# Kernel optimization log

Measured on AMD Instinct MI355X. Metric: run time of the kernel, lower is better.

The kernel has to match this reference:

```python
import jax, jax.numpy as jnp
import numpy as np

N_NODES = 100000
N_EDGES = 1600000
D_IN = 64
D_HID = 64
D_OUT = 64


def _sage_conv(x, src, dst, n_nodes, W_l, b_l, W_r):
    # mean aggregation of source features at destination nodes
    msgs = x[src]  # [E, F] gather
    agg = jax.ops.segment_sum(msgs, dst, num_segments=n_nodes)
    cnt = jax.ops.segment_sum(jnp.ones((src.shape[0],), x.dtype), dst, num_segments=n_nodes)
    mean = agg / jnp.maximum(cnt, 1.0)[:, None]  # nodes with no in-edges -> 0
    # out = lin_l(mean) + lin_r(x); lin_l has bias, lin_r does not (PyG default)
    return mean @ W_l.T + b_l + x @ W_r.T


def setup_inputs() -> dict:
    key = jax.random.key(0)
    ks = jax.random.split(key, 8)
    x = jax.random.normal(ks[0], (N_NODES, D_IN), dtype=jnp.float32)
    edge_index = jax.random.randint(ks[1], (2, N_EDGES), 0, N_NODES, dtype=jnp.int64) if jax.config.jax_enable_x64 else jax.random.randint(ks[1], (2, N_EDGES), 0, N_NODES, dtype=jnp.int32)
    s1 = 1.0 / np.sqrt(D_IN)
    s2 = 1.0 / np.sqrt(D_HID)
    W1_l = jax.random.uniform(ks[2], (D_HID, D_IN), jnp.float32, -s1, s1)
    b1_l = jax.random.uniform(ks[3], (D_HID,), jnp.float32, -s1, s1)
    W1_r = jax.random.uniform(ks[4], (D_HID, D_IN), jnp.float32, -s1, s1)
    W2_l = jax.random.uniform(ks[5], (D_OUT, D_HID), jnp.float32, -s2, s2)
    b2_l = jax.random.uniform(ks[6], (D_OUT,), jnp.float32, -s2, s2)
    W2_r = jax.random.uniform(ks[7], (D_OUT, D_HID), jnp.float32, -s2, s2)
    return {"x": x, "edge_index": edge_index, "W1_l": W1_l, "b1_l": b1_l, "W1_r": W1_r,
            "W2_l": W2_l, "b2_l": b2_l, "W2_r": W2_r}


def reference(x, edge_index, W1_l, b1_l, W1_r, W2_l, b2_l, W2_r):
    src, dst = edge_index[0], edge_index[1]
    h = _sage_conv(x, src, dst, x.shape[0], W1_l, b1_l, W1_r)
    h = jax.nn.relu(h)
    out = _sage_conv(h, src, dst, x.shape[0], W2_l, b2_l, W2_r)
    return out
```

## Files before the change

### kernel.cpp

```cpp
#include <hip/hip_runtime.h>
#include <hip/hip_fp16.h>

#define N_NODES 100000
#define N_EDGES 1600000
#define D 64

#define BSHIFT 8
#define BUCK_N 256
#define NBUCK 391
#define EPB 4096
#define NBLKA 391
#define SCAN_N (NBUCK * NBLKA)
#define SCAN_B1 ((SCAN_N + 255) / 256)
#define A4_CAP 6144
#define X_OCTETS (N_NODES * D / 8)
#define CVT_BLKS ((X_OCTETS + 2048 + 511) / 512)
#define AGB (N_NODES / 32)

typedef _Float16 half8 __attribute__((ext_vector_type(8)));
typedef float floatx4 __attribute__((ext_vector_type(4)));


__device__ __forceinline__ uint4 pack8h(float4 a, float4 b) {
    __half2 h0, h1, h2, h3;
    h0.x = __float2half(a.x); h0.y = __float2half(a.y);
    h1.x = __float2half(a.z); h1.y = __float2half(a.w);
    h2.x = __float2half(b.x); h2.y = __float2half(b.y);
    h3.x = __float2half(b.z); h3.y = __float2half(b.w);
    uint4 pk;
    pk.x = *(unsigned int*)&h0; pk.y = *(unsigned int*)&h1;
    pk.z = *(unsigned int*)&h2; pk.w = *(unsigned int*)&h3;
    return pk;
}


__global__ void pre_k(const float* __restrict__ x,
                      const float* __restrict__ W1l, const float* __restrict__ W1r,
                      const float* __restrict__ W2l, const float* __restrict__ W2r,
                      const int* __restrict__ dst, int* __restrict__ histG,
                      __half* __restrict__ x16,
                      __half* __restrict__ o1l, __half* __restrict__ o1r,
                      __half* __restrict__ o2l, __half* __restrict__ o2r) {
    __shared__ int hl[512];
    int t = threadIdx.x;
    if (blockIdx.x < NBLKA) {
        hl[t] = 0;
        __syncthreads();
        int base = blockIdx.x * EPB;
#pragma unroll
        for (int r = 0; r < 8; r++) {
            int idx = base + r * 512 + t;
            if (idx < N_EDGES) atomicAdd(&hl[dst[idx] >> BSHIFT], 1);
        }
        __syncthreads();
        if (t < NBUCK) histG[t * NBLKA + blockIdx.x] = hl[t];
        return;
    }
    int i = (blockIdx.x - NBLKA) * 512 + t;
    const float* s;
    __half* d;
    int j;
    if (i < X_OCTETS) {
        s = x; d = x16; j = i * 8;
    } else {
        int k = i - X_OCTETS;
        if (k >= 2048) return;
        int arr = k >> 9;
        j = (k & 511) * 8;
        s = (arr == 0) ? W1l : (arr == 1) ? W1r : (arr == 2) ? W2l : W2r;
        d = (arr == 0) ? o1l : (arr == 1) ? o1r : (arr == 2) ? o2l : o2r;
    }
    float4 a = *(const float4*)&s[j];
    float4 b = *(const float4*)&s[j + 4];
    *(uint4*)&d[j] = pack8h(a, b);
}


__global__ void scan1_k(int* __restrict__ data, int* __restrict__ bsums, int n) {
    __shared__ int sm[256];
    int i = blockIdx.x * 256 + threadIdx.x;
    int v = (i < n) ? data[i] : 0;
    sm[threadIdx.x] = v;
    __syncthreads();
    for (int off = 1; off < 256; off <<= 1) {
        int t = (threadIdx.x >= off) ? sm[threadIdx.x - off] : 0;
        __syncthreads();
        sm[threadIdx.x] += t;
        __syncthreads();
    }
    if (i < n) data[i] = sm[threadIdx.x] - v;
    if (threadIdx.x == 255) bsums[blockIdx.x] = sm[255];
}

__global__ void scan2_k(int* __restrict__ bsums, int nb) {
    __shared__ int sm[1024];
    int v = (threadIdx.x < nb) ? bsums[threadIdx.x] : 0;
    sm[threadIdx.x] = v;
    __syncthreads();
    for (int off = 1; off < 1024; off <<= 1) {
        int t = (threadIdx.x >= off) ? sm[threadIdx.x - off] : 0;
        __syncthreads();
        sm[threadIdx.x] += t;
        __syncthreads();
    }
    if (threadIdx.x < nb) bsums[threadIdx.x] = sm[threadIdx.x];
}

__device__ __forceinline__ int hist_abs(const int* histG, const int* bsums, int idx) {
    int v = histG[idx];
    int blk = idx >> 8;
    if (blk > 0) v += bsums[blk - 1];
    return v;
}


__global__ void a3_sort_k(const int* __restrict__ src, const int* __restrict__ dst,
                          const int* __restrict__ histG, const int* __restrict__ bsums,
                          unsigned int* __restrict__ epacked, int e) {
    __shared__ int hl[512];
    __shared__ int cur[512];
    __shared__ int sc[512];
    __shared__ int gbase[NBUCK];
    __shared__ unsigned int spk[EPB];
    __shared__ unsigned short sb[EPB];
    int t = threadIdx.x;
    int blk = blockIdx.x;
    int base = blk * EPB;

    hl[t] = 0;
    __syncthreads();

    int myd[8], mys[8];
#pragma unroll
    for (int r = 0; r < 8; r++) {
        int idx = base + r * 512 + t;
        if (idx < e) {
            myd[r] = dst[idx];
            mys[r] = src[idx];
            atomicAdd(&hl[myd[r] >> BSHIFT], 1);
        } else {
            myd[r] = -1; mys[r] = 0;
        }
    }
    __syncthreads();

    int v = hl[t];
    sc[t] = v;
    __syncthreads();
    for (int off = 1; off < 512; off <<= 1) {
        int tt = (t >= off) ? sc[t - off] : 0;
        __syncthreads();
        sc[t] += tt;
        __syncthreads();
    }
    int excl = sc[t] - v;
    hl[t] = excl;
    cur[t] = excl;
    if (t < NBUCK) gbase[t] = hist_abs(histG, bsums, t * NBLKA + blk);
    __syncthreads();

#pragma unroll
    for (int r = 0; r < 8; r++) {
        if (myd[r] >= 0) {
            int b = myd[r] >> BSHIFT;
            int dl = myd[r] & (BUCK_N - 1);
            int pos = atomicAdd(&cur[b], 1);
            spk[pos] = ((unsigned)dl << 17) | (unsigned)mys[r];
            sb[pos] = (unsigned short)b;
        }
    }
    __syncthreads();

    int cnt = e - base; if (cnt > EPB) cnt = EPB;
#pragma unroll
    for (int r = 0; r < 8; r++) {
        int i = r * 512 + t;
        if (i < cnt) {
            int b = sb[i];
            epacked[gbase[b] + (i - hl[b])] = spk[i];
        }
    }
}


__global__ void a4_nodesort_k(unsigned int* __restrict__ epk,
                              const int* __restrict__ histG, const int* __restrict__ bsums,
                              int* __restrict__ row_ptr) {
    __shared__ int sorted[A4_CAP];
    __shared__ int hist[256];
    __shared__ int cur[256];
    __shared__ int sc[512];
    int b = blockIdx.x;
    int t = threadIdx.x;

    int s0 = hist_abs(histG, bsums, b * NBLKA);
    int s1 = (b == NBUCK - 1) ? N_EDGES : hist_abs(histG, bsums, (b + 1) * NBLKA);
    int cnt = s1 - s0;
    if (cnt > A4_CAP) cnt = A4_CAP;

    if (t < 256) hist[t] = 0;
    __syncthreads();

    unsigned int my[12];
    int mycnt = 0;
    for (int i = t; i < cnt; i += 512) {
        unsigned int p = epk[s0 + i];
        my[mycnt++] = p;
        atomicAdd(&hist[p >> 17], 1);
    }
    __syncthreads();

    int v = (t < 256) ? hist[t] : 0;
    sc[t] = v;
    __syncthreads();
    for (int off = 1; off < 512; off <<= 1) {
        int tt = (t >= off) ? sc[t - off] : 0;
        __syncthreads();
        sc[t] += tt;
        __syncthreads();
    }
    int start = sc[t] - v;
    if (t < 256) cur[t] = start;
    __syncthreads();

    for (int i = 0; i < mycnt; i++) {
        unsigned int p = my[i];
        int pos = atomicAdd(&cur[p >> 17], 1);
        sorted[pos] = (int)(p & 0x1FFFF);
    }
    __syncthreads();

    for (int i = t; i < cnt; i += 512) epk[s0 + i] = (unsigned int)sorted[i];

    if (t < 256) {
        int g = (b << BSHIFT) + t;
        if (g < N_NODES) row_ptr[g] = s0 + start;
    }
    if (b == NBUCK - 1 && t == 0) row_ptr[N_NODES] = N_EDGES;
}


__device__ __forceinline__ void addp(__half2* a, uint4 v) {
    const __half2* h = (const __half2*)&v;
    a[0] = __hadd2(a[0], h[0]);
    a[1] = __hadd2(a[1], h[1]);
    a[2] = __hadd2(a[2], h[2]);
    a[3] = __hadd2(a[3], h[3]);
}

__global__ void agg_gemm_k(const __half* __restrict__ feat16,
                           const int* __restrict__ row_ptr,
                           const int* __restrict__ adj,
                           const __half* __restrict__ Wl16,
                           const __half* __restrict__ Wr16,
                           const float* __restrict__ bl,
                           float* __restrict__ out32,
                           __half* __restrict__ out16,
                           int do_relu) {
    __shared__ __half mt[32 * 64];
    int t = threadIdx.x;
    int lane = t & 63;
    int w = t >> 6;
    int fp = lane & 7;
    int gl = lane & 56;
    int nloc = w * 8 + (lane >> 3);
    int node = blockIdx.x * 32 + nloc;
    const uint4* f16 = (const uint4*)feat16;

    int fcol = lane & 15;
    int quad = lane >> 4;
    int f = w * 16 + fcol;
    half8 b0 = *(const half8*)(Wl16 + (size_t)f * 64 + quad * 8);
    half8 b1 = *(const half8*)(Wl16 + (size_t)f * 64 + 32 + quad * 8);
    half8 b2 = *(const half8*)(Wr16 + (size_t)f * 64 + quad * 8);
    half8 b3 = *(const half8*)(Wr16 + (size_t)f * 64 + 32 + quad * 8);
    float bias = bl[f];

    int beg = row_ptr[node];
    int end = row_ptr[node + 1];
    __half2 z; z.x = __float2half(0.f); z.y = z.x;
    __half2 aA[4] = {z, z, z, z};
    __half2 aB[4] = {z, z, z, z};

    int e = beg;
    for (; e + 7 < end; e += 8) {
        int am = adj[e + fp];
        int n0 = __shfl(am, gl + 0);
        int n1 = __shfl(am, gl + 1);
        int n2 = __shfl(am, gl + 2);
        int n3 = __shfl(am, gl + 3);
        int n4 = __shfl(am, gl + 4);
        int n5 = __shfl(am, gl + 5);
        int n6 = __shfl(am, gl + 6);
        int n7 = __shfl(am, gl + 7);
        uint4 v0 = f16[(size_t)n0 * 8 + fp];
        uint4 v1 = f16[(size_t)n1 * 8 + fp];
        uint4 v2 = f16[(size_t)n2 * 8 + fp];
        uint4 v3 = f16[(size_t)n3 * 8 + fp];
        uint4 v4 = f16[(size_t)n4 * 8 + fp];
        uint4 v5 = f16[(size_t)n5 * 8 + fp];
        uint4 v6 = f16[(size_t)n6 * 8 + fp];
        uint4 v7 = f16[(size_t)n7 * 8 + fp];
        addp(aA, v0); addp(aB, v1); addp(aA, v2); addp(aB, v3);
        addp(aA, v4); addp(aB, v5); addp(aA, v6); addp(aB, v7);
    }
    if (e + 3 < end) {
        uint4 v0 = f16[(size_t)adj[e] * 8 + fp];
        uint4 v1 = f16[(size_t)adj[e + 1] * 8 + fp];
        uint4 v2 = f16[(size_t)adj[e + 2] * 8 + fp];
        uint4 v3 = f16[(size_t)adj[e + 3] * 8 + fp];
        addp(aA, v0); addp(aB, v1); addp(aA, v2); addp(aB, v3);
        e += 4;
    }
    for (; e < end; e++) addp(aA, f16[(size_t)adj[e] * 8 + fp]);

    int dg = end - beg;
    float inv = (dg > 1) ? 1.0f / (float)dg : 1.0f;
    float2 s0 = __half22float2(aA[0]), s1 = __half22float2(aA[1]);
    float2 s2 = __half22float2(aA[2]), s3 = __half22float2(aA[3]);
    float2 t0 = __half22float2(aB[0]), t1 = __half22float2(aB[1]);
    float2 t2 = __half22float2(aB[2]), t3 = __half22float2(aB[3]);
    float4 o0, o1;
    o0.x = (s0.x + t0.x) * inv; o0.y = (s0.y + t0.y) * inv;
    o0.z = (s1.x + t1.x) * inv; o0.w = (s1.y + t1.y) * inv;
    o1.x = (s2.x + t2.x) * inv; o1.y = (s2.y + t2.y) * inv;
    o1.z = (s3.x + t3.x) * inv; o1.w = (s3.y + t3.y) * inv;
    *(uint4*)&mt[(size_t)nloc * 64 + 8 * (fp ^ (nloc & 7))] = pack8h(o0, o1);
    __syncthreads();

#pragma unroll
    for (int tile = 0; tile < 2; tile++) {
        int row = tile * 16 + fcol;
        half8 a0 = *(const half8*)&mt[(size_t)row * 64 + 8 * (quad ^ (row & 7))];
        half8 a1 = *(const half8*)&mt[(size_t)row * 64 + 8 * ((4 + quad) ^ (row & 7))];
        size_t frow = ((size_t)blockIdx.x * 32 + row) * 64 + quad * 8;
        half8 a2 = *(const half8*)(feat16 + frow);
        half8 a3 = *(const half8*)(feat16 + frow + 32);

        floatx4 acc = {0.f, 0.f, 0.f, 0.f};
        acc = __builtin_amdgcn_mfma_f32_16x16x32_f16(a0, b0, acc, 0, 0, 0);
        acc = __builtin_amdgcn_mfma_f32_16x16x32_f16(a1, b1, acc, 0, 0, 0);
        acc = __builtin_amdgcn_mfma_f32_16x16x32_f16(a2, b2, acc, 0, 0, 0);
        acc = __builtin_amdgcn_mfma_f32_16x16x32_f16(a3, b3, acc, 0, 0, 0);

#pragma unroll
        for (int r = 0; r < 4; r++) {
            int node2 = blockIdx.x * 32 + tile * 16 + quad * 4 + r;
            float v = acc[r] + bias;
            if (do_relu) v = fmaxf(v, 0.f);
            if (out32) out32[(size_t)node2 * 64 + f] = v;
            if (out16) out16[(size_t)node2 * 64 + f] = __float2half(v);
        }
    }
}

extern "C" void kernel_launch(void* const* d_in, const int* in_sizes, int n_in,
                              void* d_out, int out_size, void* d_ws, size_t ws_size,
                              hipStream_t stream) {
    const float* x   = (const float*)d_in[0];
    const int*   ei  = (const int*)d_in[1];
    const float* W1l = (const float*)d_in[2];
    const float* b1l = (const float*)d_in[3];
    const float* W1r = (const float*)d_in[4];
    const float* W2l = (const float*)d_in[5];
    const float* b2l = (const float*)d_in[6];
    const float* W2r = (const float*)d_in[7];
    float* out = (float*)d_out;

    const int* src = ei;
    const int* dst = ei + N_EDGES;

    __half* x16   = (__half*)d_ws;
    __half* h16   = x16 + (size_t)N_NODES * D;
    __half* w1l16 = h16 + (size_t)N_NODES * D;
    __half* w1r16 = w1l16 + 4096;
    __half* w2l16 = w1r16 + 4096;
    __half* w2r16 = w2l16 + 4096;
    int*   histG = (int*)(w2r16 + 4096);
    int*   bsums = histG + SCAN_N;
    int*   row_ptr = bsums + 1024;
    unsigned int* epk = (unsigned int*)(row_ptr + N_NODES + 2);

    pre_k<<<NBLKA + CVT_BLKS, 512, 0, stream>>>(x, W1l, W1r, W2l, W2r, dst, histG,
                                                x16, w1l16, w1r16, w2l16, w2r16);

    scan1_k<<<SCAN_B1, 256, 0, stream>>>(histG, bsums, SCAN_N);
    scan2_k<<<1, 1024, 0, stream>>>(bsums, SCAN_B1);
    a3_sort_k<<<NBLKA, 512, 0, stream>>>(src, dst, histG, bsums, epk, N_EDGES);
    a4_nodesort_k<<<NBUCK, 512, 0, stream>>>(epk, histG, bsums, row_ptr);

    agg_gemm_k<<<AGB, 256, 0, stream>>>(x16, row_ptr, (const int*)epk,
                                        w1l16, w1r16, b1l,
                                        (float*)nullptr, h16, 1);
    agg_gemm_k<<<AGB, 256, 0, stream>>>(h16, row_ptr, (const int*)epk,
                                        w2l16, w2r16, b2l,
                                        out, (__half*)nullptr, 0);
}
```

Measured before the change: 196.9 us.

## Replace two-pass bucket sort CSR build with atomic degree count and scatter

Swaps the two-level radix-style bucket sort (per-block bucket histograms, a scan over a 391x391 histogram, a local bucket sort and a per-bucket node sort) for a simpler CSR build. The new path counts per-node degree with global atomics, scans it to get row_ptr, and scatters src indices into adjacency slots via global atomicAdd cursors. This drops shared-memory sorting passes and the large histogram scan, but adds heavy global atomic contention across 1.6M edges. Neighbor order within a row also becomes nondeterministic, so fp16 sums may vary slightly from run to run.

```diff
diff --git a/kernel.cpp b/kernel.cpp
--- a/kernel.cpp
+++ b/kernel.cpp
@@ -5,16 +5,11 @@
 #define N_EDGES 1600000
 #define D 64
 
-#define BSHIFT 8
-#define BUCK_N 256
-#define NBUCK 391
 #define EPB 4096
 #define NBLKA 391
-#define SCAN_N (NBUCK * NBLKA)
-#define SCAN_B1 ((SCAN_N + 255) / 256)
-#define A4_CAP 6144
 #define X_OCTETS (N_NODES * D / 8)
 #define CVT_BLKS ((X_OCTETS + 2048 + 511) / 512)
+#define SCAN_BLKS ((N_NODES + 255) / 256)
 #define AGB (N_NODES / 32)
 
 typedef _Float16 half8 __attribute__((ext_vector_type(8)));
@@ -37,23 +32,18 @@
 __global__ void pre_k(const float* __restrict__ x,
                       const float* __restrict__ W1l, const float* __restrict__ W1r,
                       const float* __restrict__ W2l, const float* __restrict__ W2r,
-                      const int* __restrict__ dst, int* __restrict__ histG,
+                      const int* __restrict__ dst, int* __restrict__ deg,
                       __half* __restrict__ x16,
                       __half* __restrict__ o1l, __half* __restrict__ o1r,
                       __half* __restrict__ o2l, __half* __restrict__ o2r) {
-    __shared__ int hl[512];
     int t = threadIdx.x;
     if (blockIdx.x < NBLKA) {
-        hl[t] = 0;
-        __syncthreads();
         int base = blockIdx.x * EPB;
 #pragma unroll
         for (int r = 0; r < 8; r++) {
             int idx = base + r * 512 + t;
-            if (idx < N_EDGES) atomicAdd(&hl[dst[idx] >> BSHIFT], 1);
+            if (idx < N_EDGES) atomicAdd(&deg[dst[idx]], 1);
         }
-        __syncthreads();
-        if (t < NBUCK) histG[t * NBLKA + blockIdx.x] = hl[t];
         return;
     }
     int i = (blockIdx.x - NBLKA) * 512 + t;
@@ -106,137 +96,30 @@
     if (threadIdx.x < nb) bsums[threadIdx.x] = sm[threadIdx.x];
 }
 
-__device__ __forceinline__ int hist_abs(const int* histG, const int* bsums, int idx) {
-    int v = histG[idx];
-    int blk = idx >> 8;
-    if (blk > 0) v += bsums[blk - 1];
-    return v;
-}
-
-
-__global__ void a3_sort_k(const int* __restrict__ src, const int* __restrict__ dst,
-                          const int* __restrict__ histG, const int* __restrict__ bsums,
-                          unsigned int* __restrict__ epacked, int e) {
-    __shared__ int hl[512];
-    __shared__ int cur[512];
-    __shared__ int sc[512];
-    __shared__ int gbase[NBUCK];
-    __shared__ unsigned int spk[EPB];
-    __shared__ unsigned short sb[EPB];
-    int t = threadIdx.x;
-    int blk = blockIdx.x;
-    int base = blk * EPB;
-
-    hl[t] = 0;
-    __syncthreads();
-
-    int myd[8], mys[8];
-#pragma unroll
-    for (int r = 0; r < 8; r++) {
-        int idx = base + r * 512 + t;
-        if (idx < e) {
-            myd[r] = dst[idx];
-            mys[r] = src[idx];
-            atomicAdd(&hl[myd[r] >> BSHIFT], 1);
-        } else {
-            myd[r] = -1; mys[r] = 0;
-        }
-    }
-    __syncthreads();
-
-    int v = hl[t];
-    sc[t] = v;
-    __syncthreads();
-    for (int off = 1; off < 512; off <<= 1) {
-        int tt = (t >= off) ? sc[t - off] : 0;
-        __syncthreads();
-        sc[t] += tt;
-        __syncthreads();
-    }
-    int excl = sc[t] - v;
-    hl[t] = excl;
-    cur[t] = excl;
-    if (t < NBUCK) gbase[t] = hist_abs(histG, bsums, t * NBLKA + blk);
-    __syncthreads();
-
-#pragma unroll
-    for (int r = 0; r < 8; r++) {
-        if (myd[r] >= 0) {
-            int b = myd[r] >> BSHIFT;
-            int dl = myd[r] & (BUCK_N - 1);
-            int pos = atomicAdd(&cur[b], 1);
-            spk[pos] = ((unsigned)dl << 17) | (unsigned)mys[r];
-            sb[pos] = (unsigned short)b;
-        }
-    }
-    __syncthreads();
-
-    int cnt = e - base; if (cnt > EPB) cnt = EPB;
-#pragma unroll
-    for (int r = 0; r < 8; r++) {
-        int i = r * 512 + t;
-        if (i < cnt) {
-            int b = sb[i];
-            epacked[gbase[b] + (i - hl[b])] = spk[i];
-        }
-    }
-}
-
-
-__global__ void a4_nodesort_k(unsigned int* __restrict__ epk,
-                              const int* __restrict__ histG, const int* __restrict__ bsums,
-                              int* __restrict__ row_ptr) {
-    __shared__ int sorted[A4_CAP];
-    __shared__ int hist[256];
-    __shared__ int cur[256];
-    __shared__ int sc[512];
-    int b = blockIdx.x;
-    int t = threadIdx.x;
-
-    int s0 = hist_abs(histG, bsums, b * NBLKA);
-    int s1 = (b == NBUCK - 1) ? N_EDGES : hist_abs(histG, bsums, (b + 1) * NBLKA);
-    int cnt = s1 - s0;
-    if (cnt > A4_CAP) cnt = A4_CAP;
-
-    if (t < 256) hist[t] = 0;
-    __syncthreads();
-
-    unsigned int my[12];
-    int mycnt = 0;
-    for (int i = t; i < cnt; i += 512) {
-        unsigned int p = epk[s0 + i];
-        my[mycnt++] = p;
-        atomicAdd(&hist[p >> 17], 1);
-    }
-    __syncthreads();
-
-    int v = (t < 256) ? hist[t] : 0;
-    sc[t] = v;
-    __syncthreads();
-    for (int off = 1; off < 512; off <<= 1) {
-        int tt = (t >= off) ? sc[t - off] : 0;
-        __syncthreads();
-        sc[t] += tt;
-        __syncthreads();
-    }
-    int start = sc[t] - v;
-    if (t < 256) cur[t] = start;
-    __syncthreads();
-
-    for (int i = 0; i < mycnt; i++) {
-        unsigned int p = my[i];
-        int pos = atomicAdd(&cur[p >> 17], 1);
-        sorted[pos] = (int)(p & 0x1FFFF);
-    }
-    __syncthreads();
-
-    for (int i = t; i < cnt; i += 512) epk[s0 + i] = (unsigned int)sorted[i];
-
-    if (t < 256) {
-        int g = (b << BSHIFT) + t;
-        if (g < N_NODES) row_ptr[g] = s0 + start;
-    }
-    if (b == NBUCK - 1 && t == 0) row_ptr[N_NODES] = N_EDGES;
+
+__global__ void fin_k(const int* __restrict__ deg, const int* __restrict__ bsums,
+                      int* __restrict__ row_ptr, int* __restrict__ cur) {
+    int i = blockIdx.x * 256 + threadIdx.x;
+    if (i < N_NODES) {
+        int v = deg[i];
+        if (blockIdx.x > 0) v += bsums[blockIdx.x - 1];
+        row_ptr[i] = v;
+        cur[i] = v;
+    }
+    if (blockIdx.x == 0 && threadIdx.x == 0) row_ptr[N_NODES] = N_EDGES;
+}
+
+
+__global__ void scat_k(const int4* __restrict__ src4, const int4* __restrict__ dst4,
+                       int* __restrict__ cur, int* __restrict__ adj) {
+    int i = blockIdx.x * 256 + threadIdx.x;
+    if (i >= N_EDGES / 4) return;
+    int4 s = src4[i];
+    int4 d = dst4[i];
+    adj[atomicAdd(&cur[d.x], 1)] = s.x;
+    adj[atomicAdd(&cur[d.y], 1)] = s.y;
+    adj[atomicAdd(&cur[d.z], 1)] = s.z;
+    adj[atomicAdd(&cur[d.w], 1)] = s.w;
 }
 
 
@@ -376,23 +259,28 @@
     __half* w1r16 = w1l16 + 4096;
     __half* w2l16 = w1r16 + 4096;
     __half* w2r16 = w2l16 + 4096;
-    int*   histG = (int*)(w2r16 + 4096);
-    int*   bsums = histG + SCAN_N;
-    int*   row_ptr = bsums + 1024;
-    unsigned int* epk = (unsigned int*)(row_ptr + N_NODES + 2);
-
-    pre_k<<<NBLKA + CVT_BLKS, 512, 0, stream>>>(x, W1l, W1r, W2l, W2r, dst, histG,
+    int*   deg    = (int*)(w2r16 + 4096);
+    int*   bsums  = deg + N_NODES;
+    int*   row_ptr = bsums + 512;
+    int*   cur    = row_ptr + N_NODES + 1;
+    int*   adj    = cur + N_NODES;
+
+    hipMemsetAsync(deg, 0, (size_t)N_NODES * sizeof(int), stream);
+
+    pre_k<<<NBLKA + CVT_BLKS, 512, 0, stream>>>(x, W1l, W1r, W2l, W2r, dst, deg,
                                                 x16, w1l16, w1r16, w2l16, w2r16);
 
-    scan1_k<<<SCAN_B1, 256, 0, stream>>>(histG, bsums, SCAN_N);
-    scan2_k<<<1, 1024, 0, stream>>>(bsums, SCAN_B1);
-    a3_sort_k<<<NBLKA, 512, 0, stream>>>(src, dst, histG, bsums, epk, N_EDGES);
-    a4_nodesort_k<<<NBUCK, 512, 0, stream>>>(epk, histG, bsums, row_ptr);
-
-    agg_gemm_k<<<AGB, 256, 0, stream>>>(x16, row_ptr, (const int*)epk,
+    scan1_k<<<SCAN_BLKS, 256, 0, stream>>>(deg, bsums, N_NODES);
+    scan2_k<<<1, 1024, 0, stream>>>(bsums, SCAN_BLKS);
+    fin_k<<<SCAN_BLKS, 256, 0, stream>>>(deg, bsums, row_ptr, cur);
+
+    scat_k<<<(N_EDGES / 4 + 255) / 256, 256, 0, stream>>>(
+        (const int4*)src, (const int4*)dst, cur, adj);
+
+    agg_gemm_k<<<AGB, 256, 0, stream>>>(x16, row_ptr, adj,
                                         w1l16, w1r16, b1l,
                                         (float*)nullptr, h16, 1);
-    agg_gemm_k<<<AGB, 256, 0, stream>>>(h16, row_ptr, (const int*)epk,
+    agg_gemm_k<<<AGB, 256, 0, stream>>>(h16, row_ptr, adj,
                                         w2l16, w2r16, b2l,
                                         out, (__half*)nullptr, 0);
 }
```

New measurement: 357.5 us. +81.6%, slower.

## Unroll neighbor gather to 16 edges, defer weight loads, stage fp16 output stores

Applied to the files above, without the earlier changes.

The edge-gather loop now handles 16 neighbors per iteration, so more independent feature loads are in flight at once. Weight and bias fragment loads move after the aggregation to lower register pressure during the gather. The fp16 output is staged through shared memory and written back as coalesced 16-byte stores instead of scattered 2-byte stores. The cost is higher register use in the gather loop and two extra barriers in the output path.

```diff
diff --git a/kernel.cpp b/kernel.cpp
--- a/kernel.cpp
+++ b/kernel.cpp
@@ -267,15 +267,6 @@
     int node = blockIdx.x * 32 + nloc;
     const uint4* f16 = (const uint4*)feat16;
 
-    int fcol = lane & 15;
-    int quad = lane >> 4;
-    int f = w * 16 + fcol;
-    half8 b0 = *(const half8*)(Wl16 + (size_t)f * 64 + quad * 8);
-    half8 b1 = *(const half8*)(Wl16 + (size_t)f * 64 + 32 + quad * 8);
-    half8 b2 = *(const half8*)(Wr16 + (size_t)f * 64 + quad * 8);
-    half8 b3 = *(const half8*)(Wr16 + (size_t)f * 64 + 32 + quad * 8);
-    float bias = bl[f];
-
     int beg = row_ptr[node];
     int end = row_ptr[node + 1];
     __half2 z; z.x = __float2half(0.f); z.y = z.x;
@@ -283,6 +274,46 @@
     __half2 aB[4] = {z, z, z, z};
 
     int e = beg;
+    for (; e + 15 < end; e += 16) {
+        int amA = adj[e + fp];
+        int amB = adj[e + 8 + fp];
+        int n0 = __shfl(amA, gl + 0);
+        int n1 = __shfl(amA, gl + 1);
+        int n2 = __shfl(amA, gl + 2);
+        int n3 = __shfl(amA, gl + 3);
+        int n4 = __shfl(amA, gl + 4);
+        int n5 = __shfl(amA, gl + 5);
+        int n6 = __shfl(amA, gl + 6);
+        int n7 = __shfl(amA, gl + 7);
+        int n8  = __shfl(amB, gl + 0);
+        int n9  = __shfl(amB, gl + 1);
+        int n10 = __shfl(amB, gl + 2);
+        int n11 = __shfl(amB, gl + 3);
+        int n12 = __shfl(amB, gl + 4);
+        int n13 = __shfl(amB, gl + 5);
+        int n14 = __shfl(amB, gl + 6);
+        int n15 = __shfl(amB, gl + 7);
+        uint4 v0  = f16[(size_t)n0 * 8 + fp];
+        uint4 v1  = f16[(size_t)n1 * 8 + fp];
+        uint4 v2  = f16[(size_t)n2 * 8 + fp];
+        uint4 v3  = f16[(size_t)n3 * 8 + fp];
+        uint4 v4  = f16[(size_t)n4 * 8 + fp];
+        uint4 v5  = f16[(size_t)n5 * 8 + fp];
+        uint4 v6  = f16[(size_t)n6 * 8 + fp];
+        uint4 v7  = f16[(size_t)n7 * 8 + fp];
+        uint4 v8  = f16[(size_t)n8 * 8 + fp];
+        uint4 v9  = f16[(size_t)n9 * 8 + fp];
+        uint4 v10 = f16[(size_t)n10 * 8 + fp];
+        uint4 v11 = f16[(size_t)n11 * 8 + fp];
+        uint4 v12 = f16[(size_t)n12 * 8 + fp];
+        uint4 v13 = f16[(size_t)n13 * 8 + fp];
+        uint4 v14 = f16[(size_t)n14 * 8 + fp];
+        uint4 v15 = f16[(size_t)n15 * 8 + fp];
+        addp(aA, v0);  addp(aB, v1);  addp(aA, v2);  addp(aB, v3);
+        addp(aA, v4);  addp(aB, v5);  addp(aA, v6);  addp(aB, v7);
+        addp(aA, v8);  addp(aB, v9);  addp(aA, v10); addp(aB, v11);
+        addp(aA, v12); addp(aB, v13); addp(aA, v14); addp(aB, v15);
+    }
     for (; e + 7 < end; e += 8) {
         int am = adj[e + fp];
         int n0 = __shfl(am, gl + 0);
@@ -328,6 +359,16 @@
     *(uint4*)&mt[(size_t)nloc * 64 + 8 * (fp ^ (nloc & 7))] = pack8h(o0, o1);
     __syncthreads();
 
+    int fcol = lane & 15;
+    int quad = lane >> 4;
+    int f = w * 16 + fcol;
+    half8 b0 = *(const half8*)(Wl16 + (size_t)f * 64 + quad * 8);
+    half8 b1 = *(const half8*)(Wl16 + (size_t)f * 64 + 32 + quad * 8);
+    half8 b2 = *(const half8*)(Wr16 + (size_t)f * 64 + quad * 8);
+    half8 b3 = *(const half8*)(Wr16 + (size_t)f * 64 + 32 + quad * 8);
+    float bias = bl[f];
+
+    __half ores[8];
 #pragma unroll
     for (int tile = 0; tile < 2; tile++) {
         int row = tile * 16 + fcol;
@@ -349,8 +390,19 @@
             float v = acc[r] + bias;
             if (do_relu) v = fmaxf(v, 0.f);
             if (out32) out32[(size_t)node2 * 64 + f] = v;
-            if (out16) out16[(size_t)node2 * 64 + f] = __float2half(v);
+            ores[tile * 4 + r] = __float2half(v);
         }
+    }
+
+    if (out16) {
+        __syncthreads();
+#pragma unroll
+        for (int tile = 0; tile < 2; tile++)
+#pragma unroll
+            for (int r = 0; r < 4; r++)
+                mt[(size_t)(tile * 16 + quad * 4 + r) * 64 + f] = ores[tile * 4 + r];
+        __syncthreads();
+        *(uint4*)&out16[(size_t)node * 64 + fp * 8] = *(uint4*)&mt[(size_t)nloc * 64 + fp * 8];
     }
 }
 
```

Result: no change. 198.2 us (+0.6%).
